# Kernel tuning notes

Measured on AMD Instinct MI355X. Metric: run time of the kernel, lower is better.

The kernel has to match this reference:

```python
import jax, jax.numpy as jnp
import numpy as np

# locally-connected layer dims (padding='valid', stride 1)
FH, FW = 3, 3
SR, SC = 1, 1
H, W, FIN, FOUT = 32, 32, 64, 64
OH = (H - FH) // SR + 1  # 30
OW = (W - FW) // SC + 1  # 30


def _patches(X):
    # X: [N, H, W, FIN] -> [N, OH*OW, FH*FW*FIN], flatten order (fh, fw, fin)
    # matches tf.reshape(X[:, i:i+fh, j:j+fw, :], (N, fh*fw*fin))
    ps = [X[:, di:di + OH * SR:SR, dj:dj + OW * SC:SC, :]
          for di in range(FH) for dj in range(FW)]  # each [N, OH, OW, FIN]
    p = jnp.stack(ps, axis=3)  # [N, OH, OW, FH*FW, FIN]
    return p.reshape(p.shape[0], OH * OW, FH * FW * FIN)


def setup_inputs() -> dict:
    key = jax.random.key(0)
    k1, k2 = jax.random.split(key)
    X = jax.random.normal(k1, (128, H, W, FIN), dtype=jnp.float32)
    # init='sqrt_fan_in': uniform(-1/sqrt(h*w*fin), 1/sqrt(h*w*fin))
    scale = 1.0 / np.sqrt(H * W * FIN)
    filters = jax.random.uniform(k2, (OH * OW, FH * FW * FIN, FOUT),
                                 dtype=jnp.float32, minval=-scale, maxval=scale)
    return {"X": X, "filters": filters}


def reference(X, filters):
    # per-location (unshared) batched matmul:
    # patches [N, L, K] x filters [L, K, FOUT] -> [N, L, FOUT]
    p = _patches(X)
    out = jnp.einsum('nlk,lkf->nlf', p, filters)
    return out.reshape(X.shape[0], OH, OW, FOUT)
```

## Files before the change

### kernel.cpp

```cpp
#include <hip/hip_runtime.h>
#include <hip/hip_bf16.h>
#include <stdint.h>


typedef __attribute__((ext_vector_type(4))) float  f32x4;
typedef __attribute__((ext_vector_type(8))) short  short8;
typedef __attribute__((ext_vector_type(4))) short  short4v;

#define BOFF 16384

__device__ __forceinline__ uint32_t swz_addr(uint32_t row, uint32_t inrow) {
    uint32_t chunk = inrow >> 4;
    uint32_t rem   = inrow & 15u;
    return row * 128u + (((chunk ^ row ^ (row >> 3)) & 7u) << 4) + rem;
}

__device__ __forceinline__ short f2bf(float x) {
    __hip_bfloat16 h = __float2bfloat16(x);
    short r;
    __builtin_memcpy(&r, &h, 2);
    return r;
}

__global__ __launch_bounds__(256)
void lc_mfma_kernel(const float* __restrict__ X,
                    const float* __restrict__ Fl,
                    float* __restrict__ Out) {
    __shared__ __align__(16) unsigned char lds[2][24576];

    const int orig = blockIdx.x;
    const int xcd  = orig & 7;
    const int idx  = orig >> 3;
    const int l    = (xcd < 4 ? xcd * 113 : 452 + (xcd - 4) * 112) + idx;

    const int oi = l / 30;
    const int oj = l % 30;
    const int tid  = threadIdx.x;
    const int lane = tid & 63;
    const int wave = tid >> 6;

    f32x4 acc[2][4];
#pragma unroll
    for (int m = 0; m < 2; ++m)
#pragma unroll
        for (int n = 0; n < 4; ++n)
            acc[m][n] = f32x4{0.f, 0.f, 0.f, 0.f};

    const int ar = tid >> 2;
    const int aq = tid & 3;
    const int fq = tid & 15;
    const int k0 = (tid >> 4) * 4;

    const float* Fb = Fl + (size_t)l * (576 * 64);

    float4 av[8];
    float4 bv[4];

#define ISSUE_LOADS(S)                                                          \
    do {                                                                        \
        const int di_ = (S) / 3, dj_ = (S) % 3;                                 \
        const int h_ = oi + di_, w_ = oj + dj_;                                 \
        const float* a0_ = X + (((size_t)ar * 32 + h_) * 32 + w_) * 64 + aq*16; \
        const float* a1_ = a0_ + (size_t)64 * 32 * 32 * 64;                     \
        av[0] = ((const float4*)a0_)[0]; av[1] = ((const float4*)a0_)[1];       \
        av[2] = ((const float4*)a0_)[2]; av[3] = ((const float4*)a0_)[3];       \
        av[4] = ((const float4*)a1_)[0]; av[5] = ((const float4*)a1_)[1];       \
        av[6] = ((const float4*)a1_)[2]; av[7] = ((const float4*)a1_)[3];       \
        const float* b_ = Fb + (size_t)(S) * 4096 + (size_t)k0 * 64 + fq * 4;   \
        bv[0] = *(const float4*)(b_);       bv[1] = *(const float4*)(b_ + 64);  \
        bv[2] = *(const float4*)(b_ + 128); bv[3] = *(const float4*)(b_ + 192); \
    } while (0)

#define WRITE_LDS(BUF)                                                          \
    do {                                                                        \
        unsigned char* L_ = lds[BUF];                                           \
        _Pragma("unroll")                                                       \
        for (int it = 0; it < 2; ++it) {                                        \
            const float4 v0 = av[it*4+0], v1 = av[it*4+1];                      \
            const float4 v2 = av[it*4+2], v3 = av[it*4+3];                      \
            short8 p0, p1;                                                      \
            p0[0]=f2bf(v0.x); p0[1]=f2bf(v0.y); p0[2]=f2bf(v0.z); p0[3]=f2bf(v0.w); \
            p0[4]=f2bf(v1.x); p0[5]=f2bf(v1.y); p0[6]=f2bf(v1.z); p0[7]=f2bf(v1.w); \
            p1[0]=f2bf(v2.x); p1[1]=f2bf(v2.y); p1[2]=f2bf(v2.z); p1[3]=f2bf(v2.w); \
            p1[4]=f2bf(v3.x); p1[5]=f2bf(v3.y); p1[6]=f2bf(v3.z); p1[7]=f2bf(v3.w); \
            *(short8*)&L_[swz_addr(it*64 + ar, aq*32 + 0 )] = p0;               \
            *(short8*)&L_[swz_addr(it*64 + ar, aq*32 + 16)] = p1;               \
        }                                                                       \
        const short4v c0 = { f2bf(bv[0].x), f2bf(bv[1].x), f2bf(bv[2].x), f2bf(bv[3].x) }; \
        const short4v c1 = { f2bf(bv[0].y), f2bf(bv[1].y), f2bf(bv[2].y), f2bf(bv[3].y) }; \
        const short4v c2 = { f2bf(bv[0].z), f2bf(bv[1].z), f2bf(bv[2].z), f2bf(bv[3].z) }; \
        const short4v c3 = { f2bf(bv[0].w), f2bf(bv[1].w), f2bf(bv[2].w), f2bf(bv[3].w) }; \
        *(short4v*)&L_[BOFF + swz_addr(fq*4 + 0, k0*2)] = c0;                   \
        *(short4v*)&L_[BOFF + swz_addr(fq*4 + 1, k0*2)] = c1;                   \
        *(short4v*)&L_[BOFF + swz_addr(fq*4 + 2, k0*2)] = c2;                   \
        *(short4v*)&L_[BOFF + swz_addr(fq*4 + 3, k0*2)] = c3;                   \
    } while (0)

    ISSUE_LOADS(0);
    WRITE_LDS(0);

    const int mb   = wave * 32;
    const int rsel = lane & 15;
    const int ksel = (lane >> 4) * 16;

#pragma unroll 1
    for (int s = 0; s < 9; ++s) {
        if (s < 8) ISSUE_LOADS(s + 1);

        __syncthreads();

        const unsigned char* L = lds[s & 1];
#pragma unroll
        for (int kk = 0; kk < 2; ++kk) {
            const uint32_t inrow = (uint32_t)(kk * 64 + ksel);
            const short8 a0 = *(const short8*)&L[swz_addr(mb + rsel,      inrow)];
            const short8 a1 = *(const short8*)&L[swz_addr(mb + 16 + rsel, inrow)];
            const short8 b0 = *(const short8*)&L[BOFF + swz_addr(     rsel, inrow)];
            const short8 b1 = *(const short8*)&L[BOFF + swz_addr(16 + rsel, inrow)];
            const short8 b2 = *(const short8*)&L[BOFF + swz_addr(32 + rsel, inrow)];
            const short8 b3 = *(const short8*)&L[BOFF + swz_addr(48 + rsel, inrow)];
            acc[0][0] = __builtin_amdgcn_mfma_f32_16x16x32_bf16(a0, b0, acc[0][0], 0, 0, 0);
            acc[0][1] = __builtin_amdgcn_mfma_f32_16x16x32_bf16(a0, b1, acc[0][1], 0, 0, 0);
            acc[0][2] = __builtin_amdgcn_mfma_f32_16x16x32_bf16(a0, b2, acc[0][2], 0, 0, 0);
            acc[0][3] = __builtin_amdgcn_mfma_f32_16x16x32_bf16(a0, b3, acc[0][3], 0, 0, 0);
            acc[1][0] = __builtin_amdgcn_mfma_f32_16x16x32_bf16(a1, b0, acc[1][0], 0, 0, 0);
            acc[1][1] = __builtin_amdgcn_mfma_f32_16x16x32_bf16(a1, b1, acc[1][1], 0, 0, 0);
            acc[1][2] = __builtin_amdgcn_mfma_f32_16x16x32_bf16(a1, b2, acc[1][2], 0, 0, 0);
            acc[1][3] = __builtin_amdgcn_mfma_f32_16x16x32_bf16(a1, b3, acc[1][3], 0, 0, 0);
        }

        if (s < 8) WRITE_LDS((s + 1) & 1);
    }

    const int col = lane & 15;
    const int rb  = (lane >> 4) * 4;
#pragma unroll
    for (int m = 0; m < 2; ++m)
#pragma unroll
        for (int n = 0; n < 4; ++n)
#pragma unroll
            for (int i = 0; i < 4; ++i) {
                const int row = wave * 32 + m * 16 + rb + i;
                const int f   = n * 16 + col;
                Out[((size_t)row * 900 + l) * 64 + f] = acc[m][n][i];
            }
}

extern "C" void kernel_launch(void* const* d_in, const int* in_sizes, int n_in,
                              void* d_out, int out_size, void* d_ws, size_t ws_size,
                              hipStream_t stream) {
    const float* X  = (const float*)d_in[0];
    const float* Fl = (const float*)d_in[1];
    float* Out = (float*)d_out;
    lc_mfma_kernel<<<dim3(900), dim3(256), 0, stream>>>(X, Fl, Out);
}
```

Measured before the change: 40.53 us.

## Double block size to 512 threads with one 16-row MFMA tile per wave

Each block now uses 512 threads (8 waves) instead of 256. Each wave computes a 16x64 output tile instead of 32x64, and each thread loads one batch row of X instead of two. Only the upper 256 threads load and convert the filter slice. The aim is more memory-level parallelism and latency hiding per location. The cost is that each wave reloads the B fragments from LDS for half as many MFMAs, and half the threads sit idle during the filter staging.

```diff
diff --git a/kernel.cpp b/kernel.cpp
--- a/kernel.cpp
+++ b/kernel.cpp
@@ -22,7 +22,7 @@
     return r;
 }
 
-__global__ __launch_bounds__(256)
+__global__ __launch_bounds__(512, 6)
 void lc_mfma_kernel(const float* __restrict__ X,
                     const float* __restrict__ Fl,
                     float* __restrict__ Out) {
@@ -39,67 +39,62 @@
     const int lane = tid & 63;
     const int wave = tid >> 6;
 
-    f32x4 acc[2][4];
+    f32x4 acc[4];
 #pragma unroll
-    for (int m = 0; m < 2; ++m)
-#pragma unroll
-        for (int n = 0; n < 4; ++n)
-            acc[m][n] = f32x4{0.f, 0.f, 0.f, 0.f};
+    for (int n = 0; n < 4; ++n)
+        acc[n] = f32x4{0.f, 0.f, 0.f, 0.f};
 
     const int ar = tid >> 2;
     const int aq = tid & 3;
     const int fq = tid & 15;
-    const int k0 = (tid >> 4) * 4;
+    const int k0 = ((tid >> 4) & 15) * 4;
+    const bool bthread = (tid >= 256);
 
     const float* Fb = Fl + (size_t)l * (576 * 64);
 
-    float4 av[8];
+    float4 av[4];
     float4 bv[4];
 
 #define ISSUE_LOADS(S)                                                          \
     do {                                                                        \
         const int di_ = (S) / 3, dj_ = (S) % 3;                                 \
         const int h_ = oi + di_, w_ = oj + dj_;                                 \
-        const float* a0_ = X + (((size_t)ar * 32 + h_) * 32 + w_) * 64 + aq*16; \
-        const float* a1_ = a0_ + (size_t)64 * 32 * 32 * 64;                     \
-        av[0] = ((const float4*)a0_)[0]; av[1] = ((const float4*)a0_)[1];       \
-        av[2] = ((const float4*)a0_)[2]; av[3] = ((const float4*)a0_)[3];       \
-        av[4] = ((const float4*)a1_)[0]; av[5] = ((const float4*)a1_)[1];       \
-        av[6] = ((const float4*)a1_)[2]; av[7] = ((const float4*)a1_)[3];       \
-        const float* b_ = Fb + (size_t)(S) * 4096 + (size_t)k0 * 64 + fq * 4;   \
-        bv[0] = *(const float4*)(b_);       bv[1] = *(const float4*)(b_ + 64);  \
-        bv[2] = *(const float4*)(b_ + 128); bv[3] = *(const float4*)(b_ + 192); \
+        const float* a_ = X + (((size_t)ar * 32 + h_) * 32 + w_) * 64 + aq*16;  \
+        av[0] = ((const float4*)a_)[0]; av[1] = ((const float4*)a_)[1];         \
+        av[2] = ((const float4*)a_)[2]; av[3] = ((const float4*)a_)[3];         \
+        if (bthread) {                                                          \
+            const float* b_ = Fb + (size_t)(S) * 4096 + (size_t)k0 * 64 + fq*4; \
+            bv[0] = *(const float4*)(b_);       bv[1] = *(const float4*)(b_ + 64);  \
+            bv[2] = *(const float4*)(b_ + 128); bv[3] = *(const float4*)(b_ + 192); \
+        }                                                                       \
     } while (0)
 
 #define WRITE_LDS(BUF)                                                          \
     do {                                                                        \
         unsigned char* L_ = lds[BUF];                                           \
-        _Pragma("unroll")                                                       \
-        for (int it = 0; it < 2; ++it) {                                        \
-            const float4 v0 = av[it*4+0], v1 = av[it*4+1];                      \
-            const float4 v2 = av[it*4+2], v3 = av[it*4+3];                      \
-            short8 p0, p1;                                                      \
-            p0[0]=f2bf(v0.x); p0[1]=f2bf(v0.y); p0[2]=f2bf(v0.z); p0[3]=f2bf(v0.w); \
-            p0[4]=f2bf(v1.x); p0[5]=f2bf(v1.y); p0[6]=f2bf(v1.z); p0[7]=f2bf(v1.w); \
-            p1[0]=f2bf(v2.x); p1[1]=f2bf(v2.y); p1[2]=f2bf(v2.z); p1[3]=f2bf(v2.w); \
-            p1[4]=f2bf(v3.x); p1[5]=f2bf(v3.y); p1[6]=f2bf(v3.z); p1[7]=f2bf(v3.w); \
-            *(short8*)&L_[swz_addr(it*64 + ar, aq*32 + 0 )] = p0;               \
-            *(short8*)&L_[swz_addr(it*64 + ar, aq*32 + 16)] = p1;               \
+        short8 p0, p1;                                                          \
+        p0[0]=f2bf(av[0].x); p0[1]=f2bf(av[0].y); p0[2]=f2bf(av[0].z); p0[3]=f2bf(av[0].w); \
+        p0[4]=f2bf(av[1].x); p0[5]=f2bf(av[1].y); p0[6]=f2bf(av[1].z); p0[7]=f2bf(av[1].w); \
+        p1[0]=f2bf(av[2].x); p1[1]=f2bf(av[2].y); p1[2]=f2bf(av[2].z); p1[3]=f2bf(av[2].w); \
+        p1[4]=f2bf(av[3].x); p1[5]=f2bf(av[3].y); p1[6]=f2bf(av[3].z); p1[7]=f2bf(av[3].w); \
+        *(short8*)&L_[swz_addr(ar, aq*32 + 0 )] = p0;                           \
+        *(short8*)&L_[swz_addr(ar, aq*32 + 16)] = p1;                           \
+        if (bthread) {                                                          \
+            const short4v c0 = { f2bf(bv[0].x), f2bf(bv[1].x), f2bf(bv[2].x), f2bf(bv[3].x) }; \
+            const short4v c1 = { f2bf(bv[0].y), f2bf(bv[1].y), f2bf(bv[2].y), f2bf(bv[3].y) }; \
+            const short4v c2 = { f2bf(bv[0].z), f2bf(bv[1].z), f2bf(bv[2].z), f2bf(bv[3].z) }; \
+            const short4v c3 = { f2bf(bv[0].w), f2bf(bv[1].w), f2bf(bv[2].w), f2bf(bv[3].w) }; \
+            *(short4v*)&L_[BOFF + swz_addr(fq*4 + 0, k0*2)] = c0;               \
+            *(short4v*)&L_[BOFF + swz_addr(fq*4 + 1, k0*2)] = c1;               \
+            *(short4v*)&L_[BOFF + swz_addr(fq*4 + 2, k0*2)] = c2;               \
+            *(short4v*)&L_[BOFF + swz_addr(fq*4 + 3, k0*2)] = c3;               \
         }                                                                       \
-        const short4v c0 = { f2bf(bv[0].x), f2bf(bv[1].x), f2bf(bv[2].x), f2bf(bv[3].x) }; \
-        const short4v c1 = { f2bf(bv[0].y), f2bf(bv[1].y), f2bf(bv[2].y), f2bf(bv[3].y) }; \
-        const short4v c2 = { f2bf(bv[0].z), f2bf(bv[1].z), f2bf(bv[2].z), f2bf(bv[3].z) }; \
-        const short4v c3 = { f2bf(bv[0].w), f2bf(bv[1].w), f2bf(bv[2].w), f2bf(bv[3].w) }; \
-        *(short4v*)&L_[BOFF + swz_addr(fq*4 + 0, k0*2)] = c0;                   \
-        *(short4v*)&L_[BOFF + swz_addr(fq*4 + 1, k0*2)] = c1;                   \
-        *(short4v*)&L_[BOFF + swz_addr(fq*4 + 2, k0*2)] = c2;                   \
-        *(short4v*)&L_[BOFF + swz_addr(fq*4 + 3, k0*2)] = c3;                   \
     } while (0)
 
     ISSUE_LOADS(0);
     WRITE_LDS(0);
 
-    const int mb   = wave * 32;
+    const int mb   = wave * 16;
     const int rsel = lane & 15;
     const int ksel = (lane >> 4) * 16;
 
@@ -113,20 +108,15 @@
 #pragma unroll
         for (int kk = 0; kk < 2; ++kk) {
             const uint32_t inrow = (uint32_t)(kk * 64 + ksel);
-            const short8 a0 = *(const short8*)&L[swz_addr(mb + rsel,      inrow)];
-            const short8 a1 = *(const short8*)&L[swz_addr(mb + 16 + rsel, inrow)];
+            const short8 a0 = *(const short8*)&L[swz_addr(mb + rsel, inrow)];
             const short8 b0 = *(const short8*)&L[BOFF + swz_addr(     rsel, inrow)];
             const short8 b1 = *(const short8*)&L[BOFF + swz_addr(16 + rsel, inrow)];
             const short8 b2 = *(const short8*)&L[BOFF + swz_addr(32 + rsel, inrow)];
             const short8 b3 = *(const short8*)&L[BOFF + swz_addr(48 + rsel, inrow)];
-            acc[0][0] = __builtin_amdgcn_mfma_f32_16x16x32_bf16(a0, b0, acc[0][0], 0, 0, 0);
-            acc[0][1] = __builtin_amdgcn_mfma_f32_16x16x32_bf16(a0, b1, acc[0][1], 0, 0, 0);
-            acc[0][2] = __builtin_amdgcn_mfma_f32_16x16x32_bf16(a0, b2, acc[0][2], 0, 0, 0);
-            acc[0][3] = __builtin_amdgcn_mfma_f32_16x16x32_bf16(a0, b3, acc[0][3], 0, 0, 0);
-            acc[1][0] = __builtin_amdgcn_mfma_f32_16x16x32_bf16(a1, b0, acc[1][0], 0, 0, 0);
-            acc[1][1] = __builtin_amdgcn_mfma_f32_16x16x32_bf16(a1, b1, acc[1][1], 0, 0, 0);
-            acc[1][2] = __builtin_amdgcn_mfma_f32_16x16x32_bf16(a1, b2, acc[1][2], 0, 0, 0);
-            acc[1][3] = __builtin_amdgcn_mfma_f32_16x16x32_bf16(a1, b3, acc[1][3], 0, 0, 0);
+            acc[0] = __builtin_amdgcn_mfma_f32_16x16x32_bf16(a0, b0, acc[0], 0, 0, 0);
+            acc[1] = __builtin_amdgcn_mfma_f32_16x16x32_bf16(a0, b1, acc[1], 0, 0, 0);
+            acc[2] = __builtin_amdgcn_mfma_f32_16x16x32_bf16(a0, b2, acc[2], 0, 0, 0);
+            acc[3] = __builtin_amdgcn_mfma_f32_16x16x32_bf16(a0, b3, acc[3], 0, 0, 0);
         }
 
         if (s < 8) WRITE_LDS((s + 1) & 1);
@@ -135,15 +125,13 @@
     const int col = lane & 15;
     const int rb  = (lane >> 4) * 4;
 #pragma unroll
-    for (int m = 0; m < 2; ++m)
+    for (int n = 0; n < 4; ++n)
 #pragma unroll
-        for (int n = 0; n < 4; ++n)
-#pragma unroll
-            for (int i = 0; i < 4; ++i) {
-                const int row = wave * 32 + m * 16 + rb + i;
-                const int f   = n * 16 + col;
-                Out[((size_t)row * 900 + l) * 64 + f] = acc[m][n][i];
-            }
+        for (int i = 0; i < 4; ++i) {
+            const int row = mb + rb + i;
+            const int f   = n * 16 + col;
+            Out[((size_t)row * 900 + l) * 64 + f] = acc[n][i];
+        }
 }
 
 extern "C" void kernel_launch(void* const* d_in, const int* in_sizes, int n_in,
@@ -152,5 +140,5 @@
     const float* X  = (const float*)d_in[0];
     const float* Fl = (const float*)d_in[1];
     float* Out = (float*)d_out;
-    lc_mfma_kernel<<<dim3(900), dim3(256), 0, stream>>>(X, Fl, Out);
+    lc_mfma_kernel<<<dim3(900), dim3(512), 0, stream>>>(X, Fl, Out);
 }
```

Result: slower. 123.6 us (+205.1%).
